# Optimization experiments

Measured on AMD Instinct MI355X. Metric: run time of the kernel, lower is better.

The kernel has to match this reference:

```python
import jax, jax.numpy as jnp
import numpy as np

B, N, PATCH_DIM, TEXT_DIM, HIDDEN = 32, 4096, 1024, 768, 512


def setup_inputs() -> dict:
    key = jax.random.key(0)
    k = jax.random.split(key, 6)
    return {
        "patches": jax.random.normal(k[0], (B, N, PATCH_DIM), dtype=jnp.float32),
        "text": jax.random.normal(k[1], (B, TEXT_DIM), dtype=jnp.float32),
        "W_patch": jax.random.normal(k[2], (HIDDEN, PATCH_DIM), dtype=jnp.float32) * (PATCH_DIM ** -0.5),
        "b_patch": jax.random.normal(k[3], (HIDDEN,), dtype=jnp.float32) * 0.01,
        "W_text": jax.random.normal(k[4], (HIDDEN, TEXT_DIM), dtype=jnp.float32) * (TEXT_DIM ** -0.5),
        "b_text": jax.random.normal(k[5], (HIDDEN,), dtype=jnp.float32) * 0.01,
    }


def reference(patches, text, W_patch, b_patch, W_text, b_text):
    # t = text_proj(text): [B, H]
    t = text @ W_text.T + b_text
    # Algebraic reassociation of einsum('bnh,bh->bn', patches @ W_patch.T + b_patch, t):
    #   fold W_patch into t -> v: [B, patch_dim], then contract with patches directly.
    v = jnp.einsum('bh,hd->bd', t, W_patch)          # [B, patch_dim]
    scores = jnp.einsum('bnd,bd->bn', patches, v)    # [B, N]
    scores = scores + (t @ b_patch)[:, None]         # bias term of patch_proj
    return scores
```

## Files before the change

kernel.cpp:

```cpp
#include <hip/hip_runtime.h>

#define B_DIM 32
#define N_DIM 4096
#define PATCH_DIM 1024
#define TEXT_DIM 768
#define HIDDEN 512

typedef float f32x4 __attribute__((ext_vector_type(4)));

__device__ __forceinline__ float dot4(f32x4 a, f32x4 b) {
    return a.x * b.x + a.y * b.y + a.z * b.z + a.w * b.w;
}

__global__ __launch_bounds__(256) void text_proj_kernel(
    const float* __restrict__ text,
    const float* __restrict__ W_text,
    const float* __restrict__ b_text,
    float* __restrict__ t_out)
{
    const int b    = blockIdx.x;
    const int lane = threadIdx.x & 63;
    const int hbase = blockIdx.y * 64 + (threadIdx.x >> 6) * 16;

    const f32x4* tx4 = (const f32x4*)(text + (size_t)b * TEXT_DIM);
    const f32x4 t0 = tx4[lane], t1 = tx4[lane + 64], t2 = tx4[lane + 128];

    #pragma unroll 2
    for (int i = 0; i < 16; ++i) {
        const int h = hbase + i;
        const f32x4* wr = (const f32x4*)(W_text + (size_t)h * TEXT_DIM);
        float s = dot4(t0, wr[lane]) + dot4(t1, wr[lane + 64])
                + dot4(t2, wr[lane + 128]);
        #pragma unroll
        for (int off = 32; off; off >>= 1)
            s += __shfl_xor(s, off, 64);
        if (lane == 0)
            t_out[(size_t)b * HIDDEN + h] = s + b_text[h];
    }
}

__global__ __launch_bounds__(256) void fold_kernel(
    const float* __restrict__ t,
    const float* __restrict__ W_patch,
    const float* __restrict__ b_patch,
    float* __restrict__ v,
    float* __restrict__ bias_out)
{
    const int b   = blockIdx.x;
    const int dc  = blockIdx.y;
    const int tid = threadIdx.x;

    __shared__ float t_sh[HIDDEN];
    t_sh[tid]       = t[(size_t)b * HIDDEN + tid];
    t_sh[tid + 256] = t[(size_t)b * HIDDEN + tid + 256];
    __syncthreads();

    const int d = dc * 256 + tid;
    const float* wp = W_patch + d;

    float a0 = 0.f, a1 = 0.f, a2 = 0.f, a3 = 0.f;
    #pragma unroll 4
    for (int h = 0; h < HIDDEN; h += 4) {
        a0 = fmaf(t_sh[h + 0], wp[(size_t)(h + 0) * PATCH_DIM], a0);
        a1 = fmaf(t_sh[h + 1], wp[(size_t)(h + 1) * PATCH_DIM], a1);
        a2 = fmaf(t_sh[h + 2], wp[(size_t)(h + 2) * PATCH_DIM], a2);
        a3 = fmaf(t_sh[h + 3], wp[(size_t)(h + 3) * PATCH_DIM], a3);
    }
    v[(size_t)b * PATCH_DIM + d] = (a0 + a1) + (a2 + a3);

    if (dc == 0) {
        float partial = t_sh[tid] * b_patch[tid]
                      + t_sh[tid + 256] * b_patch[tid + 256];
        #pragma unroll
        for (int off = 32; off; off >>= 1)
            partial += __shfl_xor(partial, off, 64);
        __shared__ float wsum[4];
        if ((tid & 63) == 0) wsum[tid >> 6] = partial;
        __syncthreads();
        if (tid == 0)
            bias_out[b] = (wsum[0] + wsum[1]) + (wsum[2] + wsum[3]);
    }
}

__global__ __launch_bounds__(256) void score_kernel(
    const float* __restrict__ patches,
    const float* __restrict__ v,
    const float* __restrict__ bias,
    float* __restrict__ out)
{
    const int lane = threadIdx.x & 63;
    const int g    = blockIdx.x * 4 + (threadIdx.x >> 6);
    const int b    = g >> 8;
    const int row0 = g << 4;

    const f32x4* vv = (const f32x4*)(v + (size_t)b * PATCH_DIM);
    const f32x4 v0 = vv[lane], v1 = vv[lane + 64],
                v2 = vv[lane + 128], v3 = vv[lane + 192];
    const float bs = bias[b];

    for (int i = 0; i < 16; i += 4) {
        const f32x4* p0 = (const f32x4*)(patches + (size_t)(row0 + i + 0) * PATCH_DIM);
        const f32x4* p1 = (const f32x4*)(patches + (size_t)(row0 + i + 1) * PATCH_DIM);
        const f32x4* p2 = (const f32x4*)(patches + (size_t)(row0 + i + 2) * PATCH_DIM);
        const f32x4* p3 = (const f32x4*)(patches + (size_t)(row0 + i + 3) * PATCH_DIM);

        f32x4 a00 = __builtin_nontemporal_load(p0 + lane);
        f32x4 a01 = __builtin_nontemporal_load(p0 + lane + 64);
        f32x4 a02 = __builtin_nontemporal_load(p0 + lane + 128);
        f32x4 a03 = __builtin_nontemporal_load(p0 + lane + 192);
        f32x4 a10 = __builtin_nontemporal_load(p1 + lane);
        f32x4 a11 = __builtin_nontemporal_load(p1 + lane + 64);
        f32x4 a12 = __builtin_nontemporal_load(p1 + lane + 128);
        f32x4 a13 = __builtin_nontemporal_load(p1 + lane + 192);
        f32x4 a20 = __builtin_nontemporal_load(p2 + lane);
        f32x4 a21 = __builtin_nontemporal_load(p2 + lane + 64);
        f32x4 a22 = __builtin_nontemporal_load(p2 + lane + 128);
        f32x4 a23 = __builtin_nontemporal_load(p2 + lane + 192);
        f32x4 a30 = __builtin_nontemporal_load(p3 + lane);
        f32x4 a31 = __builtin_nontemporal_load(p3 + lane + 64);
        f32x4 a32 = __builtin_nontemporal_load(p3 + lane + 128);
        f32x4 a33 = __builtin_nontemporal_load(p3 + lane + 192);

        float s0 = dot4(a00, v0) + dot4(a01, v1) + dot4(a02, v2) + dot4(a03, v3);
        float s1 = dot4(a10, v0) + dot4(a11, v1) + dot4(a12, v2) + dot4(a13, v3);
        float s2 = dot4(a20, v0) + dot4(a21, v1) + dot4(a22, v2) + dot4(a23, v3);
        float s3 = dot4(a30, v0) + dot4(a31, v1) + dot4(a32, v2) + dot4(a33, v3);

        #pragma unroll
        for (int off = 32; off; off >>= 1) {
            s0 += __shfl_xor(s0, off, 64);
            s1 += __shfl_xor(s1, off, 64);
            s2 += __shfl_xor(s2, off, 64);
            s3 += __shfl_xor(s3, off, 64);
        }

        if (lane == 0) {
            f32x4 o = { s0 + bs, s1 + bs, s2 + bs, s3 + bs };
            *(f32x4*)(out + row0 + i) = o;
        }
    }
}

extern "C" void kernel_launch(void* const* d_in, const int* in_sizes, int n_in,
                              void* d_out, int out_size, void* d_ws, size_t ws_size,
                              hipStream_t stream) {
    const float* patches = (const float*)d_in[0];
    const float* text    = (const float*)d_in[1];
    const float* W_patch = (const float*)d_in[2];
    const float* b_patch = (const float*)d_in[3];
    const float* W_text  = (const float*)d_in[4];
    const float* b_text  = (const float*)d_in[5];
    float* out = (float*)d_out;

    float* t_ws    = (float*)d_ws;
    float* v_ws    = t_ws + B_DIM * HIDDEN;
    float* bias_ws = v_ws + B_DIM * PATCH_DIM;

    text_proj_kernel<<<dim3(B_DIM, 8), 256, 0, stream>>>(text, W_text, b_text, t_ws);
    fold_kernel<<<dim3(B_DIM, 4), 256, 0, stream>>>(t_ws, W_patch, b_patch, v_ws, bias_ws);
    score_kernel<<<2048, 256, 0, stream>>>(patches, v_ws, bias_ws, out);
}
```

Baseline: 112.5 us.

## Fuse text projection into fold kernel and double-buffer patch loads in score kernel

```diff
diff --git a/kernel.cpp b/kernel.cpp
--- a/kernel.cpp
+++ b/kernel.cpp
@@ -12,35 +12,10 @@
     return a.x * b.x + a.y * b.y + a.z * b.z + a.w * b.w;
 }
 
-__global__ __launch_bounds__(256) void text_proj_kernel(
+__global__ __launch_bounds__(256) void prep_kernel(
     const float* __restrict__ text,
     const float* __restrict__ W_text,
     const float* __restrict__ b_text,
-    float* __restrict__ t_out)
-{
-    const int b    = blockIdx.x;
-    const int lane = threadIdx.x & 63;
-    const int hbase = blockIdx.y * 64 + (threadIdx.x >> 6) * 16;
-
-    const f32x4* tx4 = (const f32x4*)(text + (size_t)b * TEXT_DIM);
-    const f32x4 t0 = tx4[lane], t1 = tx4[lane + 64], t2 = tx4[lane + 128];
-
-    #pragma unroll 2
-    for (int i = 0; i < 16; ++i) {
-        const int h = hbase + i;
-        const f32x4* wr = (const f32x4*)(W_text + (size_t)h * TEXT_DIM);
-        float s = dot4(t0, wr[lane]) + dot4(t1, wr[lane + 64])
-                + dot4(t2, wr[lane + 128]);
-        #pragma unroll
-        for (int off = 32; off; off >>= 1)
-            s += __shfl_xor(s, off, 64);
-        if (lane == 0)
-            t_out[(size_t)b * HIDDEN + h] = s + b_text[h];
-    }
-}
-
-__global__ __launch_bounds__(256) void fold_kernel(
-    const float* __restrict__ t,
     const float* __restrict__ W_patch,
     const float* __restrict__ b_patch,
     float* __restrict__ v,
@@ -51,13 +26,29 @@
     const int tid = threadIdx.x;
 
     __shared__ float t_sh[HIDDEN];
-    t_sh[tid]       = t[(size_t)b * HIDDEN + tid];
-    t_sh[tid + 256] = t[(size_t)b * HIDDEN + tid + 256];
+
+    const f32x4* tx4 = (const f32x4*)(text + (size_t)b * TEXT_DIM);
+    #pragma unroll
+    for (int hh = 0; hh < 2; ++hh) {
+        const int h = tid + hh * 256;
+        const f32x4* w = (const f32x4*)(W_text + (size_t)h * TEXT_DIM);
+        f32x4 acc0 = {0,0,0,0}, acc1 = {0,0,0,0};
+        #pragma unroll 4
+        for (int j = 0; j < TEXT_DIM / 4; j += 2) {
+            f32x4 a0 = tx4[j],     w0 = w[j];
+            f32x4 a1 = tx4[j + 1], w1 = w[j + 1];
+            acc0.x += a0.x * w0.x; acc0.y += a0.y * w0.y;
+            acc0.z += a0.z * w0.z; acc0.w += a0.w * w0.w;
+            acc1.x += a1.x * w1.x; acc1.y += a1.y * w1.y;
+            acc1.z += a1.z * w1.z; acc1.w += a1.w * w1.w;
+        }
+        t_sh[h] = (acc0.x + acc0.y) + (acc0.z + acc0.w)
+                + (acc1.x + acc1.y) + (acc1.z + acc1.w) + b_text[h];
+    }
     __syncthreads();
 
     const int d = dc * 256 + tid;
     const float* wp = W_patch + d;
-
     float a0 = 0.f, a1 = 0.f, a2 = 0.f, a3 = 0.f;
     #pragma unroll 4
     for (int h = 0; h < HIDDEN; h += 4) {
@@ -82,6 +73,38 @@
     }
 }
 
+__device__ __forceinline__ void load_group(
+    const float* __restrict__ patches, int row, int lane, f32x4 (&A)[16]) {
+    #pragma unroll
+    for (int r = 0; r < 4; ++r) {
+        const f32x4* p = (const f32x4*)(patches + (size_t)(row + r) * PATCH_DIM);
+        #pragma unroll
+        for (int k = 0; k < 4; ++k)
+            A[r * 4 + k] = __builtin_nontemporal_load(p + lane + 64 * k);
+    }
+}
+
+__device__ __forceinline__ void reduce_store_group(
+    const f32x4 (&A)[16], const f32x4 (&V)[4], float bs,
+    float* __restrict__ out, int row, int lane) {
+    float s0 = dot4(A[0], V[0]) + dot4(A[1], V[1]) + dot4(A[2], V[2]) + dot4(A[3], V[3]);
+    float s1 = dot4(A[4], V[0]) + dot4(A[5], V[1]) + dot4(A[6], V[2]) + dot4(A[7], V[3]);
+    float s2 = dot4(A[8], V[0]) + dot4(A[9], V[1]) + dot4(A[10], V[2]) + dot4(A[11], V[3]);
+    float s3 = dot4(A[12], V[0]) + dot4(A[13], V[1]) + dot4(A[14], V[2]) + dot4(A[15], V[3]);
+
+    #pragma unroll
+    for (int off = 32; off; off >>= 1) {
+        s0 += __shfl_xor(s0, off, 64);
+        s1 += __shfl_xor(s1, off, 64);
+        s2 += __shfl_xor(s2, off, 64);
+        s3 += __shfl_xor(s3, off, 64);
+    }
+    if (lane == 0) {
+        f32x4 o = { s0 + bs, s1 + bs, s2 + bs, s3 + bs };
+        *(f32x4*)(out + row) = o;
+    }
+}
+
 __global__ __launch_bounds__(256) void score_kernel(
     const float* __restrict__ patches,
     const float* __restrict__ v,
@@ -94,51 +117,21 @@
     const int row0 = g << 4;
 
     const f32x4* vv = (const f32x4*)(v + (size_t)b * PATCH_DIM);
-    const f32x4 v0 = vv[lane], v1 = vv[lane + 64],
-                v2 = vv[lane + 128], v3 = vv[lane + 192];
+    f32x4 V[4];
+    #pragma unroll
+    for (int k = 0; k < 4; ++k) V[k] = vv[lane + 64 * k];
     const float bs = bias[b];
 
-    for (int i = 0; i < 16; i += 4) {
-        const f32x4* p0 = (const f32x4*)(patches + (size_t)(row0 + i + 0) * PATCH_DIM);
-        const f32x4* p1 = (const f32x4*)(patches + (size_t)(row0 + i + 1) * PATCH_DIM);
-        const f32x4* p2 = (const f32x4*)(patches + (size_t)(row0 + i + 2) * PATCH_DIM);
-        const f32x4* p3 = (const f32x4*)(patches + (size_t)(row0 + i + 3) * PATCH_DIM);
+    f32x4 bufA[16], bufB[16];
 
-        f32x4 a00 = __builtin_nontemporal_load(p0 + lane);
-        f32x4 a01 = __builtin_nontemporal_load(p0 + lane + 64);
-        f32x4 a02 = __builtin_nontemporal_load(p0 + lane + 128);
-        f32x4 a03 = __builtin_nontemporal_load(p0 + lane + 192);
-        f32x4 a10 = __builtin_nontemporal_load(p1 + lane);
-        f32x4 a11 = __builtin_nontemporal_load(p1 + lane + 64);
-        f32x4 a12 = __builtin_nontemporal_load(p1 + lane + 128);
-        f32x4 a13 = __builtin_nontemporal_load(p1 + lane + 192);
-        f32x4 a20 = __builtin_nontemporal_load(p2 + lane);
-        f32x4 a21 = __builtin_nontemporal_load(p2 + lane + 64);
-        f32x4 a22 = __builtin_nontemporal_load(p2 + lane + 128);
-        f32x4 a23 = __builtin_nontemporal_load(p2 + lane + 192);
-        f32x4 a30 = __builtin_nontemporal_load(p3 + lane);
-        f32x4 a31 = __builtin_nontemporal_load(p3 + lane + 64);
-        f32x4 a32 = __builtin_nontemporal_load(p3 + lane + 128);
-        f32x4 a33 = __builtin_nontemporal_load(p3 + lane + 192);
-
-        float s0 = dot4(a00, v0) + dot4(a01, v1) + dot4(a02, v2) + dot4(a03, v3);
-        float s1 = dot4(a10, v0) + dot4(a11, v1) + dot4(a12, v2) + dot4(a13, v3);
-        float s2 = dot4(a20, v0) + dot4(a21, v1) + dot4(a22, v2) + dot4(a23, v3);
-        float s3 = dot4(a30, v0) + dot4(a31, v1) + dot4(a32, v2) + dot4(a33, v3);
-
-        #pragma unroll
-        for (int off = 32; off; off >>= 1) {
-            s0 += __shfl_xor(s0, off, 64);
-            s1 += __shfl_xor(s1, off, 64);
-            s2 += __shfl_xor(s2, off, 64);
-            s3 += __shfl_xor(s3, off, 64);
-        }
-
-        if (lane == 0) {
-            f32x4 o = { s0 + bs, s1 + bs, s2 + bs, s3 + bs };
-            *(f32x4*)(out + row0 + i) = o;
-        }
-    }
+    load_group(patches, row0 + 0, lane, bufA);
+    load_group(patches, row0 + 4, lane, bufB);
+    reduce_store_group(bufA, V, bs, out, row0 + 0, lane);
+    load_group(patches, row0 + 8, lane, bufA);
+    reduce_store_group(bufB, V, bs, out, row0 + 4, lane);
+    load_group(patches, row0 + 12, lane, bufB);
+    reduce_store_group(bufA, V, bs, out, row0 + 8, lane);
+    reduce_store_group(bufB, V, bs, out, row0 + 12, lane);
 }
 
 extern "C" void kernel_launch(void* const* d_in, const int* in_sizes, int n_in,
@@ -152,11 +145,11 @@
     const float* b_text  = (const float*)d_in[5];
     float* out = (float*)d_out;
 
-    float* t_ws    = (float*)d_ws;
-    float* v_ws    = t_ws + B_DIM * HIDDEN;
+    float* v_ws    = (float*)d_ws;
     float* bias_ws = v_ws + B_DIM * PATCH_DIM;
 
-    text_proj_kernel<<<dim3(B_DIM, 8), 256, 0, stream>>>(text, W_text, b_text, t_ws);
-    fold_kernel<<<dim3(B_DIM, 4), 256, 0, stream>>>(t_ws, W_patch, b_patch, v_ws, bias_ws);
+    prep_kernel<<<dim3(B_DIM, 4), 256, 0, stream>>>(text, W_text, b_text,
+                                                    W_patch, b_patch,
+                                                    v_ws, bias_ws);
     score_kernel<<<2048, 256, 0, stream>>>(patches, v_ws, bias_ws, out);
 }
```

Result: slower. 142.0 us (+26.2%).

## Fuse text projection and W_patch fold into one per-batch prep kernel

Applied to the files above, without the earlier changes.

```diff
diff --git a/kernel.cpp b/kernel.cpp
--- a/kernel.cpp
+++ b/kernel.cpp
@@ -12,22 +12,38 @@
     return a.x * b.x + a.y * b.y + a.z * b.z + a.w * b.w;
 }
 
-__global__ __launch_bounds__(256) void text_proj_kernel(
+__device__ __forceinline__ f32x4 fma4(f32x4 a, float s, f32x4 w) {
+    a.x = fmaf(s, w.x, a.x);
+    a.y = fmaf(s, w.y, a.y);
+    a.z = fmaf(s, w.z, a.z);
+    a.w = fmaf(s, w.w, a.w);
+    return a;
+}
+
+__global__ __launch_bounds__(1024) void prep_kernel(
     const float* __restrict__ text,
     const float* __restrict__ W_text,
     const float* __restrict__ b_text,
-    float* __restrict__ t_out)
+    const float* __restrict__ W_patch,
+    const float* __restrict__ b_patch,
+    float* __restrict__ v,
+    float* __restrict__ bias_out)
 {
     const int b    = blockIdx.x;
-    const int lane = threadIdx.x & 63;
-    const int hbase = blockIdx.y * 64 + (threadIdx.x >> 6) * 16;
+    const int tid  = threadIdx.x;
+    const int lane = tid & 63;
+    const int wid  = tid >> 6;
+
+    __shared__ float t_sh[HIDDEN];
+    __shared__ f32x4 part_sh[4][256];
+    __shared__ float wsum[16];
 
     const f32x4* tx4 = (const f32x4*)(text + (size_t)b * TEXT_DIM);
     const f32x4 t0 = tx4[lane], t1 = tx4[lane + 64], t2 = tx4[lane + 128];
 
     #pragma unroll 2
-    for (int i = 0; i < 16; ++i) {
-        const int h = hbase + i;
+    for (int i = 0; i < 32; ++i) {
+        const int h = wid * 32 + i;
         const f32x4* wr = (const f32x4*)(W_text + (size_t)h * TEXT_DIM);
         float s = dot4(t0, wr[lane]) + dot4(t1, wr[lane + 64])
                 + dot4(t2, wr[lane + 128]);
@@ -35,50 +51,50 @@
         for (int off = 32; off; off >>= 1)
             s += __shfl_xor(s, off, 64);
         if (lane == 0)
-            t_out[(size_t)b * HIDDEN + h] = s + b_text[h];
+            t_sh[h] = s + b_text[h];
     }
-}
-
-__global__ __launch_bounds__(256) void fold_kernel(
-    const float* __restrict__ t,
-    const float* __restrict__ W_patch,
-    const float* __restrict__ b_patch,
-    float* __restrict__ v,
-    float* __restrict__ bias_out)
-{
-    const int b   = blockIdx.x;
-    const int dc  = blockIdx.y;
-    const int tid = threadIdx.x;
-
-    __shared__ float t_sh[HIDDEN];
-    t_sh[tid]       = t[(size_t)b * HIDDEN + tid];
-    t_sh[tid + 256] = t[(size_t)b * HIDDEN + tid + 256];
     __syncthreads();
 
-    const int d = dc * 256 + tid;
-    const float* wp = W_patch + d;
+    const int hg    = tid >> 8;
+    const int t8    = tid & 255;
+    const int hbase = hg * 128;
 
-    float a0 = 0.f, a1 = 0.f, a2 = 0.f, a3 = 0.f;
-    #pragma unroll 4
-    for (int h = 0; h < HIDDEN; h += 4) {
-        a0 = fmaf(t_sh[h + 0], wp[(size_t)(h + 0) * PATCH_DIM], a0);
-        a1 = fmaf(t_sh[h + 1], wp[(size_t)(h + 1) * PATCH_DIM], a1);
-        a2 = fmaf(t_sh[h + 2], wp[(size_t)(h + 2) * PATCH_DIM], a2);
-        a3 = fmaf(t_sh[h + 3], wp[(size_t)(h + 3) * PATCH_DIM], a3);
+    f32x4 acc[8];
+    #pragma unroll
+    for (int k = 0; k < 8; ++k) acc[k] = (f32x4){0.f, 0.f, 0.f, 0.f};
+
+    #pragma unroll 2
+    for (int h = 0; h < 128; h += 8) {
+        #pragma unroll
+        for (int k = 0; k < 8; ++k) {
+            const int hh = hbase + h + k;
+            const f32x4 w =
+                ((const f32x4*)(W_patch + (size_t)hh * PATCH_DIM))[t8];
+            acc[k] = fma4(acc[k], t_sh[hh], w);
+        }
     }
-    v[(size_t)b * PATCH_DIM + d] = (a0 + a1) + (a2 + a3);
+    f32x4 accs = ((acc[0] + acc[1]) + (acc[2] + acc[3]))
+               + ((acc[4] + acc[5]) + (acc[6] + acc[7]));
+    part_sh[hg][t8] = accs;
+    __syncthreads();
 
-    if (dc == 0) {
-        float partial = t_sh[tid] * b_patch[tid]
-                      + t_sh[tid + 256] * b_patch[tid + 256];
+    if (hg == 0) {
+        f32x4 r = (part_sh[0][t8] + part_sh[1][t8])
+                + (part_sh[2][t8] + part_sh[3][t8]);
+        ((f32x4*)(v + (size_t)b * PATCH_DIM))[t8] = r;
+    }
+
+    float partial = (tid < HIDDEN) ? t_sh[tid] * b_patch[tid] : 0.f;
+    #pragma unroll
+    for (int off = 32; off; off >>= 1)
+        partial += __shfl_xor(partial, off, 64);
+    if (lane == 0) wsum[wid] = partial;
+    __syncthreads();
+    if (tid == 0) {
+        float s = 0.f;
         #pragma unroll
-        for (int off = 32; off; off >>= 1)
-            partial += __shfl_xor(partial, off, 64);
-        __shared__ float wsum[4];
-        if ((tid & 63) == 0) wsum[tid >> 6] = partial;
-        __syncthreads();
-        if (tid == 0)
-            bias_out[b] = (wsum[0] + wsum[1]) + (wsum[2] + wsum[3]);
+        for (int w = 0; w < 16; ++w) s += wsum[w];
+        bias_out[b] = s;
     }
 }
 
@@ -152,11 +168,10 @@
     const float* b_text  = (const float*)d_in[5];
     float* out = (float*)d_out;
 
-    float* t_ws    = (float*)d_ws;
-    float* v_ws    = t_ws + B_DIM * HIDDEN;
+    float* v_ws    = (float*)d_ws;
     float* bias_ws = v_ws + B_DIM * PATCH_DIM;
 
-    text_proj_kernel<<<dim3(B_DIM, 8), 256, 0, stream>>>(text, W_text, b_text, t_ws);
-    fold_kernel<<<dim3(B_DIM, 4), 256, 0, stream>>>(t_ws, W_patch, b_patch, v_ws, bias_ws);
+    prep_kernel<<<B_DIM, 1024, 0, stream>>>(text, W_text, b_text,
+                                            W_patch, b_patch, v_ws, bias_ws);
     score_kernel<<<2048, 256, 0, stream>>>(patches, v_ws, bias_ws, out);
 }
```

After: 131.3 us. 1.17x slower.
